# Kernel tuning notes

Measured on AMD Instinct MI355X. Metric: run time of the kernel, lower is better.

The kernel has to match this reference:

```python
import jax, jax.numpy as jnp
import numpy as np
import math

H = 8
KAPPA = 20.0
STAGES = 10
BN_EPS = 1e-5


def _l2norm(x, axis):
    return x / (1e-6 + jnp.linalg.norm(x, axis=axis, keepdims=True))


def _pmms(node, query_feature, mu0):
    # node: (b,c,n)  query_feature: (b,n,c)  mu0: (1,c,k)
    b = node.shape[0]
    mu = jnp.broadcast_to(mu0, (b, mu0.shape[1], mu0.shape[2]))

    def step(mu, _):
        z = jax.nn.softmax(KAPPA * jnp.einsum('bcn,bck->bnk', node, mu), axis=2)
        z = z / (1e-6 + z.sum(axis=1, keepdims=True))
        mu = _l2norm(jnp.einsum('bcn,bnk->bck', node, z), axis=1)
        return mu, None

    mu, _ = jax.lax.scan(step, mu, None, length=STAGES)
    mu = jax.lax.stop_gradient(mu)  # torch.no_grad in EM
    P = jax.lax.stop_gradient(
        jax.nn.softmax(jnp.einsum('bnc,bck->bnk', query_feature, mu), axis=2))
    return P, mu


def _conv2d_same(x, w):
    return jax.lax.conv_general_dilated(
        x, w, (1, 1), 'SAME', dimension_numbers=('NCHW', 'OIHW', 'NCHW'))


def _node_weight(x, cw1, cb1, g, be, cw2, cb2):
    # x: (b, n, ch) with n a perfect square
    b, n, ch = x.shape
    w = int(math.isqrt(n))
    y = x.transpose(0, 2, 1).reshape(b * ch, 1, w, w)
    y = _conv2d_same(y, cw1) + cb1[None, :, None, None]
    # eval-mode BatchNorm2d (running_mean=0, running_var=1)
    y = g[None, :, None, None] * (y / jnp.sqrt(1.0 + BN_EPS)) + be[None, :, None, None]
    y = jax.nn.relu(y)
    y = _conv2d_same(y, cw2) + cb2[None, :, None, None]
    y = jax.nn.sigmoid(y)
    y = y.reshape(b, ch, n).transpose(0, 2, 1)
    return x * y


def setup_inputs() -> dict:
    key = jax.random.key(0)
    ks = jax.random.split(key, 16)
    b, n, d = 16, 1024, 256
    s = 0.02
    mu_a = _l2norm(jax.random.normal(ks[6], (1, d, 5), jnp.float32) * math.sqrt(2.0 / 5), axis=1)
    mu_b = _l2norm(jax.random.normal(ks[7], (1, d, 2), jnp.float32) * math.sqrt(2.0 / 2), axis=1)
    return {
        'query': jax.random.normal(ks[0], (b, n, d), jnp.float32),
        'key': jax.random.normal(ks[1], (b, n, d), jnp.float32),
        'value': jax.random.normal(ks[2], (b, n), jnp.float32),
        'lamda': jax.random.uniform(ks[3], (1,), jnp.float32),
        'W0': jax.random.normal(ks[4], (d, d), jnp.float32) * s,
        'b0': jnp.zeros((d,), jnp.float32),
        'W1': jax.random.normal(ks[5], (d, d), jnp.float32) * s,
        'b1': jnp.zeros((d,), jnp.float32),
        'mu_a': mu_a,
        'mu_b': mu_b,
        'nw1_w1': jax.random.normal(ks[8], (16, 1, 3, 3), jnp.float32) * 0.1,
        'nw1_b1': jnp.zeros((16,), jnp.float32),
        'nw1_g': jnp.ones((16,), jnp.float32),
        'nw1_be': jnp.zeros((16,), jnp.float32),
        'nw1_w2': jax.random.normal(ks[9], (1, 16, 3, 3), jnp.float32) * 0.1,
        'nw1_b2': jnp.zeros((1,), jnp.float32),
        'nw2_w1': jax.random.normal(ks[10], (16, 1, 3, 3), jnp.float32) * 0.1,
        'nw2_b1': jnp.zeros((16,), jnp.float32),
        'nw2_g': jnp.ones((16,), jnp.float32),
        'nw2_be': jnp.zeros((16,), jnp.float32),
        'nw2_w2': jax.random.normal(ks[11], (1, 16, 3, 3), jnp.float32) * 0.1,
        'nw2_b2': jnp.zeros((1,), jnp.float32),
    }


def reference(query, key, value, lamda, W0, b0, W1, b1, mu_a, mu_b,
              nw1_w1, nw1_b1, nw1_g, nw1_be, nw1_w2, nw1_b2,
              nw2_w1, nw2_b1, nw2_g, nw2_be, nw2_w2, nw2_b2):
    b, n, d = query.shape
    dk = d // H
    scale = 1.0 / math.sqrt(dk)
    # linear projections, split heads: (b,H,n,dk)
    q_l = (query @ W0.T + b0).reshape(b, n, H, dk).transpose(0, 2, 1, 3)
    k_l = (key @ W1.T + b1).reshape(b, n, H, dk).transpose(0, 2, 1, 3)
    v = value[:, None, :, None]  # (b,1,n,1) broadcast over heads
    # global path: value-weighted mean key, elementwise multiply-reduce, relu
    key_global = jnp.mean(k_l * v, axis=-2, keepdims=True)  # (b,H,1,dk)
    whole = jax.nn.relu(jnp.sum(q_l * key_global, axis=-1, keepdims=True) * scale)
    whole = jnp.mean(whole, axis=-3)  # (b,n,1)
    # local path: standard softmax attention with scalar values (dropout eval=identity)
    scores = jnp.einsum('bhqd,bhkd->bhqk', q_l, k_l) * scale
    p_attn = jax.nn.softmax(scores, axis=-1)
    part = jnp.einsum('bhqk,bk->bhq', p_attn, value)[..., None]  # (b,H,n,1)
    part = jnp.mean(part, axis=-3)  # (b,n,1)
    f = (1.0 - lamda) * part + lamda * whole
    # PMMs prototype clustering
    qT = query.transpose(0, 2, 1)  # (b,c,n)
    P1, m1 = _pmms(qT, query, mu_a)   # (b,n,5), (b,c,5)
    P2, _ = _pmms(m1, query, mu_b)    # (b,n,2)
    q1 = _node_weight(P1, nw1_w1, nw1_b1, nw1_g, nw1_be, nw1_w2, nw1_b2)
    q2 = _node_weight(P2, nw2_w1, nw2_b1, nw2_g, nw2_be, nw2_w2, nw2_b2)
    # tree_drop eval=identity
    return jnp.concatenate((f, q1, q2), axis=-1)  # (b,n,8)
```

## Files before the change

### kernel.cpp

```cpp
#include <hip/hip_runtime.h>
#include <hip/hip_bf16.h>
#include <math.h>

#define NN 1024
#define ND 256
#define PSTRIDE 1288

typedef __hip_bfloat16 bf;
__device__ __forceinline__ float bf2f(bf h) { return __bfloat162float(h); }

typedef __attribute__((ext_vector_type(8))) short bf16x8;
typedef __attribute__((ext_vector_type(4))) float f32x4;

__device__ __forceinline__ float wave_reduce_sum(float v) {
#pragma unroll
    for (int off = 32; off > 0; off >>= 1) v += __shfl_down(v, off, 64);
    return v;
}
__device__ __forceinline__ float wave_allreduce_sum(float v) {
#pragma unroll
    for (int off = 1; off < 64; off <<= 1) v += __shfl_xor(v, off, 64);
    return v;
}

__global__ void zero_k(float* __restrict__ out) {
    int i = blockIdx.x * 1024 + threadIdx.x;
    out[(size_t)i * 8] = 0.f;
}

__global__ __launch_bounds__(256) void gemm2_k(
    const float* __restrict__ Aq, const float* __restrict__ Ak,
    const float* __restrict__ W0, const float* __restrict__ b0v,
    const float* __restrict__ W1, const float* __restrict__ b1v,
    bf* __restrict__ QL, bf* __restrict__ KL)
{
    const float* A; const float* Bw; const float* bias; bf* C;
    if (blockIdx.z == 0) { A = Aq; Bw = W0; bias = b0v; C = QL; }
    else                 { A = Ak; Bw = W1; bias = b1v; C = KL; }
    __shared__ short Ahi[4 * 64 * 8],  Alo[4 * 64 * 8];
    __shared__ short Bhi[16 * 64 * 8], Blo[16 * 64 * 8];
    const int t = threadIdx.x;
    const int wave = t >> 6, lane = t & 63;
    const int m0 = blockIdx.x * 64;

    f32x4 acc[4][4];
#pragma unroll
    for (int m = 0; m < 4; m++)
#pragma unroll
        for (int n = 0; n < 4; n++)
#pragma unroll
            for (int r = 0; r < 4; r++) acc[m][n][r] = 0.f;

    for (int k0 = 0; k0 < 256; k0 += 32) {
        __syncthreads();
        {
            int fm = t >> 6, ls = t & 63;
            const float* src = A + (size_t)(m0 + fm * 16 + (ls & 15)) * 256 + k0 + ((ls >> 4) * 8);
            float4 x = *(const float4*)src;
            float4 y = *(const float4*)(src + 4);
            float v[8] = {x.x, x.y, x.z, x.w, y.x, y.y, y.z, y.w};
            short h[8], l8[8];
#pragma unroll
            for (int j = 0; j < 8; j++) {
                bf hb = __float2bfloat16(v[j]);
                float hf = __bfloat162float(hb);
                bf lb = __float2bfloat16(v[j] - hf);
                h[j] = *(short*)&hb; l8[j] = *(short*)&lb;
            }
            *(bf16x8*)&Ahi[t * 8] = *(bf16x8*)h;
            *(bf16x8*)&Alo[t * 8] = *(bf16x8*)l8;
        }
#pragma unroll
        for (int i = 0; i < 4; i++) {
            int idx = t + i * 256;
            int nf = idx >> 6, ls = idx & 63;
            const float* src = Bw + (size_t)(nf * 16 + (ls & 15)) * 256 + k0 + ((ls >> 4) * 8);
            float4 x = *(const float4*)src;
            float4 y = *(const float4*)(src + 4);
            float v[8] = {x.x, x.y, x.z, x.w, y.x, y.y, y.z, y.w};
            short h[8], l8[8];
#pragma unroll
            for (int j = 0; j < 8; j++) {
                bf hb = __float2bfloat16(v[j]);
                float hf = __bfloat162float(hb);
                bf lb = __float2bfloat16(v[j] - hf);
                h[j] = *(short*)&hb; l8[j] = *(short*)&lb;
            }
            *(bf16x8*)&Bhi[idx * 8] = *(bf16x8*)h;
            *(bf16x8*)&Blo[idx * 8] = *(bf16x8*)l8;
        }
        __syncthreads();
        bf16x8 ah[4], al[4], bh[4], bl[4];
#pragma unroll
        for (int m = 0; m < 4; m++) {
            ah[m] = *(const bf16x8*)&Ahi[(m * 64 + lane) * 8];
            al[m] = *(const bf16x8*)&Alo[(m * 64 + lane) * 8];
        }
#pragma unroll
        for (int n = 0; n < 4; n++) {
            int nf = wave * 4 + n;
            bh[n] = *(const bf16x8*)&Bhi[(nf * 64 + lane) * 8];
            bl[n] = *(const bf16x8*)&Blo[(nf * 64 + lane) * 8];
        }
#pragma unroll
        for (int m = 0; m < 4; m++)
#pragma unroll
            for (int n = 0; n < 4; n++) {
                acc[m][n] = __builtin_amdgcn_mfma_f32_16x16x32_bf16(ah[m], bh[n], acc[m][n], 0, 0, 0);
                acc[m][n] = __builtin_amdgcn_mfma_f32_16x16x32_bf16(ah[m], bl[n], acc[m][n], 0, 0, 0);
                acc[m][n] = __builtin_amdgcn_mfma_f32_16x16x32_bf16(al[m], bh[n], acc[m][n], 0, 0, 0);
            }
    }
#pragma unroll
    for (int n = 0; n < 4; n++) {
        int col = (wave * 4 + n) * 16 + (lane & 15);
        float bv = bias[col];
#pragma unroll
        for (int m = 0; m < 4; m++) {
            int row = m0 + m * 16 + (lane >> 4) * 4;
#pragma unroll
            for (int r = 0; r < 4; r++) {
                bf hv = __float2bfloat16(acc[m][n][r] + bv);
                C[(size_t)(row + r) * 256 + col] = hv;
            }
        }
    }
}

__global__ __launch_bounds__(256) void attn3_k(
    const bf* __restrict__ QL, const bf* __restrict__ KL,
    const float* __restrict__ value, const float* __restrict__ lamda,
    float* __restrict__ out)
{
    const int bh = blockIdx.x; const int b = bh >> 3, h = bh & 7;
    const int t = threadIdx.x;
    const int wave = t >> 6, lane = t & 63;
    const int q0 = blockIdx.y * 256 + wave * 64;
    const float scale = 0.17677669529663687f;

    __shared__ bf Kf[128 * 32];
    __shared__ float vv[128];

    bf16x8 qf[4];
    {
        const bf* qbase = QL + ((size_t)b * NN) * ND + h * 32 + (lane >> 4) * 8;
#pragma unroll
        for (int m = 0; m < 4; m++)
            qf[m] = *(const bf16x8*)(qbase + (size_t)(q0 + m * 16 + (lane & 15)) * ND);
    }
    f32x4 lsum[4], vacc[4], wacc[4];
#pragma unroll
    for (int m = 0; m < 4; m++)
#pragma unroll
        for (int r = 0; r < 4; r++) { lsum[m][r] = 0.f; vacc[m][r] = 0.f; wacc[m][r] = 0.f; }

    const bf* kbase = KL + ((size_t)b * NN) * ND + h * 32;
    for (int kt = 0; kt < 8; kt++) {
        const int k0 = kt * 128;
        __syncthreads();
#pragma unroll
        for (int i = 0; i < 2; i++) {
            int f = t + i * 256;
            int row = ((f >> 6) << 4) + (f & 15);
            int chunk = (f >> 4) & 3;
            *(bf16x8*)&Kf[f * 8] = *(const bf16x8*)(kbase + (size_t)(k0 + row) * ND + chunk * 8);
        }
        if (t < 128) vv[t] = value[(size_t)b * NN + k0 + t];
        __syncthreads();
#pragma unroll
        for (int s = 0; s < 8; s++) {
            bf16x8 bfr = *(const bf16x8*)&Kf[(s * 64 + lane) * 8];
            float vcol = vv[s * 16 + (lane & 15)];
#pragma unroll
            for (int m = 0; m < 4; m++) {
                f32x4 acc = {0.f, 0.f, 0.f, 0.f};
                acc = __builtin_amdgcn_mfma_f32_16x16x32_bf16(qf[m], bfr, acc, 0, 0, 0);
#pragma unroll
                for (int r = 0; r < 4; r++) {
                    float sraw = acc[r];
                    float p = __expf(sraw * scale);
                    lsum[m][r] += p;
                    vacc[m][r] += p * vcol;
                    wacc[m][r] += sraw * vcol;
                }
            }
        }
    }
    const float lam = lamda[0];
#pragma unroll
    for (int m = 0; m < 4; m++)
#pragma unroll
        for (int r = 0; r < 4; r++) {
            float ls = lsum[m][r], va = vacc[m][r], wa = wacc[m][r];
#pragma unroll
            for (int off = 1; off < 16; off <<= 1) {
                ls += __shfl_xor(ls, off, 64);
                va += __shfl_xor(va, off, 64);
                wa += __shfl_xor(wa, off, 64);
            }
            if ((lane & 15) == 0) {
                int q = q0 + m * 16 + (lane >> 4) * 4 + r;
                float part = va / ls;
                float whole = fmaxf(wa * scale * (1.0f / 1024.0f), 0.f);
                float f = ((1.f - lam) * part + lam * whole) * 0.125f;
                atomicAdd(&out[((size_t)b * NN + q) * 8], f);
            }
        }
}

__global__ __launch_bounds__(256) void pmms_a_k(
    const float* __restrict__ query, const float* __restrict__ mu0a,
    const float* __restrict__ pin, float* __restrict__ pout, int stage)
{
    __shared__ float qs[64 * 260];
    __shared__ float muT[5 * 256];
    __shared__ float z_s[64][8];
    __shared__ float red[32];
    int chunk = blockIdx.x, b = blockIdx.y;
    int t = threadIdx.x;
    int wave = t >> 6, lane = t & 63;

    {
        const float* qg = query + ((size_t)b * NN + chunk * 64) * ND;
        for (int i = t; i < 4096; i += 256) {
            int row = i >> 6, c4 = (i & 63) * 4;
            *(float4*)&qs[row * 260 + c4] = *(const float4*)&qg[(size_t)row * ND + c4];
        }
    }

    if (stage == 0) {
        for (int idx = t; idx < 1280; idx += 256)
            muT[idx] = mu0a[(idx & 255) * 5 + (idx >> 8)];
    } else {
        float mr[5] = {0,0,0,0,0};
        float cs[5] = {0,0,0,0,0};
        for (int ch = 0; ch < 16; ch++) {
            const float* pb = pin + ((size_t)(b * 16 + ch)) * PSTRIDE;
#pragma unroll
            for (int k = 0; k < 5; k++) mr[k] += pb[k * 256 + t];
#pragma unroll
            for (int k = 0; k < 5; k++) cs[k] += pb[1280 + k];
        }
#pragma unroll
        for (int k = 0; k < 5; k++) mr[k] *= 1.0f / (1e-6f + cs[k]);
#pragma unroll
        for (int k = 0; k < 5; k++) {
            float s = wave_reduce_sum(mr[k] * mr[k]);
            if (lane == 0) red[wave * 5 + k] = s;
        }
        __syncthreads();
        if (t < 5) red[20 + t] = 1.0f / (1e-6f + sqrtf(red[t] + red[5 + t] + red[10 + t] + red[15 + t]));
        __syncthreads();
#pragma unroll
        for (int k = 0; k < 5; k++) muT[k * 256 + t] = mr[k] * red[20 + k];
    }
    __syncthreads();

    int n_local = t >> 2, part = t & 3;
    const float* qrow = &qs[n_local * 260 + part * 64];
    float lg[5] = {0,0,0,0,0};
#pragma unroll
    for (int c4 = 0; c4 < 64; c4 += 4) {
        float4 qv = *(const float4*)&qrow[c4];
#pragma unroll
        for (int k = 0; k < 5; k++) {
            float4 mv = *(const float4*)&muT[k * 256 + part * 64 + c4];
            lg[k] += qv.x*mv.x + qv.y*mv.y + qv.z*mv.z + qv.w*mv.w;
        }
    }
#pragma unroll
    for (int k = 0; k < 5; k++) {
        lg[k] += __shfl_xor(lg[k], 1, 64);
        lg[k] += __shfl_xor(lg[k], 2, 64);
    }
    float mx = lg[0];
#pragma unroll
    for (int k = 1; k < 5; k++) mx = fmaxf(mx, lg[k]);
    float e[5], ssum = 0.f;
#pragma unroll
    for (int k = 0; k < 5; k++) { e[k] = expf(20.0f * (lg[k] - mx)); ssum += e[k]; }
    float is = 1.0f / ssum;
    if (part == 0) {
#pragma unroll
        for (int k = 0; k < 5; k++) z_s[n_local][k] = e[k] * is;
    }
    __syncthreads();

    float pa[5] = {0,0,0,0,0};
#pragma unroll 4
    for (int nl = 0; nl < 64; nl++) {
        float qv = qs[nl * 260 + t];
        float4 z4 = *(const float4*)&z_s[nl][0];
        float z4v = z_s[nl][4];
        pa[0] += qv * z4.x; pa[1] += qv * z4.y; pa[2] += qv * z4.z;
        pa[3] += qv * z4.w; pa[4] += qv * z4v;
    }
    float* pb = pout + ((size_t)(b * 16 + chunk)) * PSTRIDE;
#pragma unroll
    for (int k = 0; k < 5; k++) pb[k * 256 + t] = pa[k];
    if (t < 5) {
        float s = 0.f;
        for (int nl = 0; nl < 64; nl++) s += z_s[nl][t];
        pb[1280 + t] = s;
    }
}

__global__ __launch_bounds__(64) void pmms_b_k(
    const float* __restrict__ pin, const float* __restrict__ mu0b,
    float* __restrict__ m1_ws, float* __restrict__ mu2_ws)
{
    int b = blockIdx.x, lane = threadIdx.x;
    float nd[5][4];
    float cs[5] = {0,0,0,0,0};
#pragma unroll
    for (int n = 0; n < 5; n++)
#pragma unroll
        for (int j = 0; j < 4; j++) nd[n][j] = 0.f;
    for (int ch = 0; ch < 16; ch++) {
        const float* pb = pin + ((size_t)(b * 16 + ch)) * PSTRIDE;
#pragma unroll
        for (int n = 0; n < 5; n++)
#pragma unroll
            for (int j = 0; j < 4; j++) nd[n][j] += pb[n * 256 + lane + 64 * j];
#pragma unroll
        for (int n = 0; n < 5; n++) cs[n] += pb[1280 + n];
    }
#pragma unroll
    for (int n = 0; n < 5; n++) {
        float inv = 1.0f / (1e-6f + cs[n]);
        float sq = 0.f;
#pragma unroll
        for (int j = 0; j < 4; j++) { nd[n][j] *= inv; sq += nd[n][j] * nd[n][j]; }
        float s = wave_allreduce_sum(sq);
        float nr = 1.0f / (1e-6f + sqrtf(s));
#pragma unroll
        for (int j = 0; j < 4; j++) {
            nd[n][j] *= nr;
            m1_ws[((size_t)b * 5 + n) * 256 + lane + 64 * j] = nd[n][j];
        }
    }
    float mu[2][4];
#pragma unroll
    for (int k = 0; k < 2; k++)
#pragma unroll
        for (int j = 0; j < 4; j++) mu[k][j] = mu0b[(lane + 64 * j) * 2 + k];
    for (int stage = 0; stage < 10; stage++) {
        float z[5][2];
        float colsum0 = 0.f, colsum1 = 0.f;
#pragma unroll
        for (int n = 0; n < 5; n++) {
            float l0 = 0.f, l1 = 0.f;
#pragma unroll
            for (int j = 0; j < 4; j++) { l0 += nd[n][j] * mu[0][j]; l1 += nd[n][j] * mu[1][j]; }
            l0 = wave_allreduce_sum(l0);
            l1 = wave_allreduce_sum(l1);
            float a0 = 20.0f * l0, a1 = 20.0f * l1;
            float mxv = fmaxf(a0, a1);
            float e0 = expf(a0 - mxv), e1 = expf(a1 - mxv);
            float inv = 1.0f / (e0 + e1);
            z[n][0] = e0 * inv; z[n][1] = e1 * inv;
            colsum0 += z[n][0]; colsum1 += z[n][1];
        }
        float i0 = 1.0f / (1e-6f + colsum0), i1 = 1.0f / (1e-6f + colsum1);
#pragma unroll
        for (int k = 0; k < 2; k++) {
            float iv = k ? i1 : i0;
            float sq = 0.f;
            float nm[4];
#pragma unroll
            for (int j = 0; j < 4; j++) {
                float v = 0.f;
#pragma unroll
                for (int n = 0; n < 5; n++) v += nd[n][j] * z[n][k];
                v *= iv;
                nm[j] = v; sq += v * v;
            }
            float s = wave_allreduce_sum(sq);
            float nr = 1.0f / (1e-6f + sqrtf(s));
#pragma unroll
            for (int j = 0; j < 4; j++) mu[k][j] = nm[j] * nr;
        }
    }
#pragma unroll
    for (int k = 0; k < 2; k++)
#pragma unroll
        for (int j = 0; j < 4; j++) mu2_ws[((size_t)b * 2 + k) * 256 + lane + 64 * j] = mu[k][j];
}

__global__ __launch_bounds__(256) void pmap_k(
    const float* __restrict__ query, const float* __restrict__ m1_ws,
    const float* __restrict__ mu2_ws, float* __restrict__ P1, float* __restrict__ P2)
{
    __shared__ float ms[7 * 256];
    int b = blockIdx.y;
    int t = threadIdx.x;
    int n = blockIdx.x * 256 + t;
    for (int idx = t; idx < 1280; idx += 256) ms[idx] = m1_ws[(size_t)b * 1280 + idx];
    for (int idx = t; idx < 512; idx += 256) ms[1280 + idx] = mu2_ws[(size_t)b * 512 + idx];
    __syncthreads();
    const float* qrow = query + ((size_t)b * NN + n) * ND;
    float lg[7] = {0,0,0,0,0,0,0};
    for (int c4 = 0; c4 < 256; c4 += 4) {
        float4 qv = *(const float4*)&qrow[c4];
#pragma unroll
        for (int k = 0; k < 7; k++) {
            float4 mv = *(const float4*)&ms[k * 256 + c4];
            lg[k] += qv.x*mv.x + qv.y*mv.y + qv.z*mv.z + qv.w*mv.w;
        }
    }
    float mx = lg[0];
#pragma unroll
    for (int k = 1; k < 5; k++) mx = fmaxf(mx, lg[k]);
    float e[5], ssum = 0.f;
#pragma unroll
    for (int k = 0; k < 5; k++) { e[k] = expf(lg[k] - mx); ssum += e[k]; }
    float is = 1.0f / ssum;
#pragma unroll
    for (int k = 0; k < 5; k++) P1[((size_t)b * 5 + k) * NN + n] = e[k] * is;
    float mx2 = fmaxf(lg[5], lg[6]);
    float e0 = expf(lg[5] - mx2), e1 = expf(lg[6] - mx2);
    float inv = 1.0f / (e0 + e1);
    P2[((size_t)b * 2 + 0) * NN + n] = e0 * inv;
    P2[((size_t)b * 2 + 1) * NN + n] = e1 * inv;
}

__global__ __launch_bounds__(1024) void nwconv_k(
    const float* __restrict__ P1, const float* __restrict__ P2,
    const float* __restrict__ w1a, const float* __restrict__ b1a,
    const float* __restrict__ ga,  const float* __restrict__ bea,
    const float* __restrict__ w2a, const float* __restrict__ b2a,
    const float* __restrict__ w1b, const float* __restrict__ b1b,
    const float* __restrict__ gb,  const float* __restrict__ beb,
    const float* __restrict__ w2b, const float* __restrict__ b2b,
    float* __restrict__ out)
{
    __shared__ float img[34 * 34];
    __shared__ float mid[16][34 * 34];
    __shared__ float w1s[144], w2s[144], bs[16], gs[16], bes[16], b2s[1];
    int ch = blockIdx.x, b = blockIdx.y;
    int t = threadIdx.x;
    int i = t >> 5, j = t & 31;
    const float* xsrc = (ch < 5) ? &P1[((size_t)b * 5 + ch) * NN]
                                 : &P2[((size_t)b * 2 + (ch - 5)) * NN];
    if (t < 144) { w1s[t] = (ch < 5 ? w1a : w1b)[t]; w2s[t] = (ch < 5 ? w2a : w2b)[t]; }
    if (t >= 256 && t < 272) {
        int y = t - 256;
        bs[y] = (ch < 5 ? b1a : b1b)[y];
        gs[y] = (ch < 5 ? ga : gb)[y];
        bes[y] = (ch < 5 ? bea : beb)[y];
    }
    if (t == 512) b2s[0] = (ch < 5 ? b2a : b2b)[0];
    for (int idx = t; idx < 1156; idx += 1024) img[idx] = 0.f;
    for (int idx = t; idx < 16 * 1156; idx += 1024) ((float*)mid)[idx] = 0.f;
    __syncthreads();
    float xv = xsrc[t];
    img[(i + 1) * 34 + (j + 1)] = xv;
    __syncthreads();
    float r[9];
#pragma unroll
    for (int dy = 0; dy < 3; dy++)
#pragma unroll
        for (int dx = 0; dx < 3; dx++)
            r[dy * 3 + dx] = img[(i + dy) * 34 + (j + dx)];
    const float bninv = rsqrtf(1.0f + 1e-5f);
#pragma unroll
    for (int oc = 0; oc < 16; oc++) {
        float a = 0.f;
#pragma unroll
        for (int q2 = 0; q2 < 9; q2++) a += w1s[oc * 9 + q2] * r[q2];
        a += bs[oc];
        a = gs[oc] * (a * bninv) + bes[oc];
        a = fmaxf(a, 0.f);
        mid[oc][(i + 1) * 34 + (j + 1)] = a;
    }
    __syncthreads();
    float acc2 = b2s[0];
#pragma unroll
    for (int oc = 0; oc < 16; oc++)
#pragma unroll
        for (int dy = 0; dy < 3; dy++)
#pragma unroll
            for (int dx = 0; dx < 3; dx++)
                acc2 += w2s[oc * 9 + dy * 3 + dx] * mid[oc][(i + dy) * 34 + (j + dx)];
    float sig = 1.0f / (1.0f + expf(-acc2));
    out[((size_t)(b * NN + t)) * 8 + 1 + ch] = xv * sig;
}

extern "C" void kernel_launch(void* const* d_in, const int* in_sizes, int n_in,
                              void* d_out, int out_size, void* d_ws, size_t ws_size,
                              hipStream_t stream) {
    const float* query = (const float*)d_in[0];
    const float* key   = (const float*)d_in[1];
    const float* value = (const float*)d_in[2];
    const float* lamda = (const float*)d_in[3];
    const float* W0 = (const float*)d_in[4];
    const float* b0 = (const float*)d_in[5];
    const float* W1 = (const float*)d_in[6];
    const float* b1 = (const float*)d_in[7];
    const float* mu_a = (const float*)d_in[8];
    const float* mu_b = (const float*)d_in[9];
    const float* nw1_w1 = (const float*)d_in[10];
    const float* nw1_b1 = (const float*)d_in[11];
    const float* nw1_g  = (const float*)d_in[12];
    const float* nw1_be = (const float*)d_in[13];
    const float* nw1_w2 = (const float*)d_in[14];
    const float* nw1_b2 = (const float*)d_in[15];
    const float* nw2_w1 = (const float*)d_in[16];
    const float* nw2_b1 = (const float*)d_in[17];
    const float* nw2_g  = (const float*)d_in[18];
    const float* nw2_be = (const float*)d_in[19];
    const float* nw2_w2 = (const float*)d_in[20];
    const float* nw2_b2 = (const float*)d_in[21];
    float* out = (float*)d_out;

    bf* QLb = (bf*)d_ws;
    bf* KLb = (bf*)((char*)d_ws + ((size_t)8 << 20));
    float* PA   = (float*)d_ws;
    float* PB   = PA + (size_t)16 * 16 * PSTRIDE;
    float* m1w  = PB + (size_t)16 * 16 * PSTRIDE;
    float* mu2w = m1w + (size_t)16 * 1280;
    float* P1w  = mu2w + (size_t)16 * 512;
    float* P2w  = P1w + (size_t)16 * 5 * 1024;

    zero_k<<<16, 1024, 0, stream>>>(out);
    gemm2_k<<<dim3(256, 1, 2), 256, 0, stream>>>(query, key, W0, b0, W1, b1, QLb, KLb);
    attn3_k<<<dim3(128, 4), 256, 0, stream>>>(QLb, KLb, value, lamda, out);
    for (int s = 0; s < 10; s++) {
        const float* pin = (s & 1) ? PA : PB;
        float* pout      = (s & 1) ? PB : PA;
        pmms_a_k<<<dim3(16, 16), 256, 0, stream>>>(query, mu_a, pin, pout, s);
    }
    pmms_b_k<<<16, 64, 0, stream>>>(PB, mu_b, m1w, mu2w);
    pmap_k<<<dim3(4, 16), 256, 0, stream>>>(query, m1w, mu2w, P1w, P2w);
    nwconv_k<<<dim3(7, 16), 1024, 0, stream>>>(P1w, P2w,
                                    nw1_w1, nw1_b1, nw1_g, nw1_be, nw1_w2, nw1_b2,
                                    nw2_w1, nw2_b1, nw2_g, nw2_be, nw2_w2, nw2_b2, out);
}
```

Measured before the change: 397.1 us.

## Fold softmax scale into Q projection, halve attention tile, split PMMs mu update

The Q projection output is pre-scaled by scale*log2(e) so the attention inner loop can use exp2 directly, and the whole-path constant becomes ln2/1024 to match. The attention kernel now gives each wave 32 queries instead of 64 and launches twice as many blocks, trading more K reloads for more occupancy. The PMMs EM loop is split into a small per-batch mu normalization kernel and a z-accumulation kernel over 32 chunks of 32 rows. The z kernel reads query straight from global memory instead of staging it in LDS, so the mu reduction is no longer repeated in every block, at the cost of twice as many kernel launches.

```diff
diff --git a/kernel.cpp b/kernel.cpp
--- a/kernel.cpp
+++ b/kernel.cpp
@@ -4,13 +4,16 @@
 
 #define NN 1024
 #define ND 256
+#define NCH 32
 #define PSTRIDE 1288
 
 typedef __hip_bfloat16 bf;
-__device__ __forceinline__ float bf2f(bf h) { return __bfloat162float(h); }
 
 typedef __attribute__((ext_vector_type(8))) short bf16x8;
 typedef __attribute__((ext_vector_type(4))) float f32x4;
+
+#define QL_ALPHA 0.25503486216f
+#define WHOLE_LN2 0.6931471805599453f
 
 __device__ __forceinline__ float wave_reduce_sum(float v) {
 #pragma unroll
@@ -34,9 +37,9 @@
     const float* __restrict__ W1, const float* __restrict__ b1v,
     bf* __restrict__ QL, bf* __restrict__ KL)
 {
-    const float* A; const float* Bw; const float* bias; bf* C;
-    if (blockIdx.z == 0) { A = Aq; Bw = W0; bias = b0v; C = QL; }
-    else                 { A = Ak; Bw = W1; bias = b1v; C = KL; }
+    const float* A; const float* Bw; const float* bias; bf* C; float alpha;
+    if (blockIdx.z == 0) { A = Aq; Bw = W0; bias = b0v; C = QL; alpha = QL_ALPHA; }
+    else                 { A = Ak; Bw = W1; bias = b1v; C = KL; alpha = 1.0f; }
     __shared__ short Ahi[4 * 64 * 8],  Alo[4 * 64 * 8];
     __shared__ short Bhi[16 * 64 * 8], Blo[16 * 64 * 8];
     const int t = threadIdx.x;
@@ -120,14 +123,14 @@
             int row = m0 + m * 16 + (lane >> 4) * 4;
 #pragma unroll
             for (int r = 0; r < 4; r++) {
-                bf hv = __float2bfloat16(acc[m][n][r] + bv);
+                bf hv = __float2bfloat16((acc[m][n][r] + bv) * alpha);
                 C[(size_t)(row + r) * 256 + col] = hv;
             }
         }
     }
 }
 
-__global__ __launch_bounds__(256) void attn3_k(
+__global__ __launch_bounds__(256) void attn4_k(
     const bf* __restrict__ QL, const bf* __restrict__ KL,
     const float* __restrict__ value, const float* __restrict__ lamda,
     float* __restrict__ out)
@@ -135,22 +138,21 @@
     const int bh = blockIdx.x; const int b = bh >> 3, h = bh & 7;
     const int t = threadIdx.x;
     const int wave = t >> 6, lane = t & 63;
-    const int q0 = blockIdx.y * 256 + wave * 64;
-    const float scale = 0.17677669529663687f;
+    const int q0 = blockIdx.y * 128 + wave * 32;
 
     __shared__ bf Kf[128 * 32];
     __shared__ float vv[128];
 
-    bf16x8 qf[4];
+    bf16x8 qf[2];
     {
         const bf* qbase = QL + ((size_t)b * NN) * ND + h * 32 + (lane >> 4) * 8;
 #pragma unroll
-        for (int m = 0; m < 4; m++)
+        for (int m = 0; m < 2; m++)
             qf[m] = *(const bf16x8*)(qbase + (size_t)(q0 + m * 16 + (lane & 15)) * ND);
     }
-    f32x4 lsum[4], vacc[4], wacc[4];
-#pragma unroll
-    for (int m = 0; m < 4; m++)
+    f32x4 lsum[2], vacc[2], wacc[2];
+#pragma unroll
+    for (int m = 0; m < 2; m++)
 #pragma unroll
         for (int r = 0; r < 4; r++) { lsum[m][r] = 0.f; vacc[m][r] = 0.f; wacc[m][r] = 0.f; }
 
@@ -172,13 +174,13 @@
             bf16x8 bfr = *(const bf16x8*)&Kf[(s * 64 + lane) * 8];
             float vcol = vv[s * 16 + (lane & 15)];
 #pragma unroll
-            for (int m = 0; m < 4; m++) {
+            for (int m = 0; m < 2; m++) {
                 f32x4 acc = {0.f, 0.f, 0.f, 0.f};
                 acc = __builtin_amdgcn_mfma_f32_16x16x32_bf16(qf[m], bfr, acc, 0, 0, 0);
 #pragma unroll
                 for (int r = 0; r < 4; r++) {
                     float sraw = acc[r];
-                    float p = __expf(sraw * scale);
+                    float p = exp2f(sraw);
                     lsum[m][r] += p;
                     vacc[m][r] += p * vcol;
                     wacc[m][r] += sraw * vcol;
@@ -188,7 +190,7 @@
     }
     const float lam = lamda[0];
 #pragma unroll
-    for (int m = 0; m < 4; m++)
+    for (int m = 0; m < 2; m++)
 #pragma unroll
         for (int r = 0; r < 4; r++) {
             float ls = lsum[m][r], va = vacc[m][r], wa = wacc[m][r];
@@ -201,106 +203,110 @@
             if ((lane & 15) == 0) {
                 int q = q0 + m * 16 + (lane >> 4) * 4 + r;
                 float part = va / ls;
-                float whole = fmaxf(wa * scale * (1.0f / 1024.0f), 0.f);
+                float whole = fmaxf(wa * (WHOLE_LN2 / 1024.0f), 0.f);
                 float f = ((1.f - lam) * part + lam * whole) * 0.125f;
                 atomicAdd(&out[((size_t)b * NN + q) * 8], f);
             }
         }
 }
 
-__global__ __launch_bounds__(256) void pmms_a_k(
+__global__ __launch_bounds__(256) void mu_k(
+    const float* __restrict__ pin, float* __restrict__ muG)
+{
+    __shared__ float red[32];
+    const int b = blockIdx.x, t = threadIdx.x;
+    const int wave = t >> 6, lane = t & 63;
+    float mr[5] = {0,0,0,0,0};
+    float cs[5] = {0,0,0,0,0};
+    for (int ch = 0; ch < NCH; ch++) {
+        const float* pb = pin + ((size_t)(b * NCH + ch)) * PSTRIDE;
+#pragma unroll
+        for (int k = 0; k < 5; k++) mr[k] += pb[k * 256 + t];
+#pragma unroll
+        for (int k = 0; k < 5; k++) cs[k] += pb[1280 + k];
+    }
+#pragma unroll
+    for (int k = 0; k < 5; k++) mr[k] *= 1.0f / (1e-6f + cs[k]);
+#pragma unroll
+    for (int k = 0; k < 5; k++) {
+        float s = wave_reduce_sum(mr[k] * mr[k]);
+        if (lane == 0) red[wave * 5 + k] = s;
+    }
+    __syncthreads();
+    if (t < 5) red[20 + t] = 1.0f / (1e-6f + sqrtf(red[t] + red[5 + t] + red[10 + t] + red[15 + t]));
+    __syncthreads();
+#pragma unroll
+    for (int k = 0; k < 5; k++)
+        muG[(size_t)b * 1280 + k * 256 + t] = mr[k] * red[20 + k];
+}
+
+__global__ __launch_bounds__(256) void zacc_k(
     const float* __restrict__ query, const float* __restrict__ mu0a,
-    const float* __restrict__ pin, float* __restrict__ pout, int stage)
-{
-    __shared__ float qs[64 * 260];
+    const float* __restrict__ muG, float* __restrict__ pout, int stage)
+{
     __shared__ float muT[5 * 256];
-    __shared__ float z_s[64][8];
-    __shared__ float red[32];
-    int chunk = blockIdx.x, b = blockIdx.y;
-    int t = threadIdx.x;
-    int wave = t >> 6, lane = t & 63;
-
-    {
-        const float* qg = query + ((size_t)b * NN + chunk * 64) * ND;
-        for (int i = t; i < 4096; i += 256) {
-            int row = i >> 6, c4 = (i & 63) * 4;
-            *(float4*)&qs[row * 260 + c4] = *(const float4*)&qg[(size_t)row * ND + c4];
-        }
-    }
+    __shared__ float z_s[32][8];
+    const int chunk = blockIdx.x, b = blockIdx.y;
+    const int t = threadIdx.x;
 
     if (stage == 0) {
         for (int idx = t; idx < 1280; idx += 256)
             muT[idx] = mu0a[(idx & 255) * 5 + (idx >> 8)];
     } else {
-        float mr[5] = {0,0,0,0,0};
-        float cs[5] = {0,0,0,0,0};
-        for (int ch = 0; ch < 16; ch++) {
-            const float* pb = pin + ((size_t)(b * 16 + ch)) * PSTRIDE;
-#pragma unroll
-            for (int k = 0; k < 5; k++) mr[k] += pb[k * 256 + t];
-#pragma unroll
-            for (int k = 0; k < 5; k++) cs[k] += pb[1280 + k];
-        }
-#pragma unroll
-        for (int k = 0; k < 5; k++) mr[k] *= 1.0f / (1e-6f + cs[k]);
+        for (int idx = t; idx < 1280; idx += 256)
+            muT[idx] = muG[(size_t)b * 1280 + idx];
+    }
+    __syncthreads();
+
+    const int n_local = t >> 3, part = t & 7;
+    {
+        const float* qrow = query + ((size_t)b * NN + chunk * 32 + n_local) * ND + part * 32;
+        float lg[5] = {0,0,0,0,0};
+#pragma unroll
+        for (int c4 = 0; c4 < 32; c4 += 4) {
+            float4 qv = *(const float4*)&qrow[c4];
+#pragma unroll
+            for (int k = 0; k < 5; k++) {
+                float4 mv = *(const float4*)&muT[k * 256 + part * 32 + c4];
+                lg[k] += qv.x*mv.x + qv.y*mv.y + qv.z*mv.z + qv.w*mv.w;
+            }
+        }
 #pragma unroll
         for (int k = 0; k < 5; k++) {
-            float s = wave_reduce_sum(mr[k] * mr[k]);
-            if (lane == 0) red[wave * 5 + k] = s;
-        }
-        __syncthreads();
-        if (t < 5) red[20 + t] = 1.0f / (1e-6f + sqrtf(red[t] + red[5 + t] + red[10 + t] + red[15 + t]));
-        __syncthreads();
-#pragma unroll
-        for (int k = 0; k < 5; k++) muT[k * 256 + t] = mr[k] * red[20 + k];
-    }
-    __syncthreads();
-
-    int n_local = t >> 2, part = t & 3;
-    const float* qrow = &qs[n_local * 260 + part * 64];
-    float lg[5] = {0,0,0,0,0};
-#pragma unroll
-    for (int c4 = 0; c4 < 64; c4 += 4) {
-        float4 qv = *(const float4*)&qrow[c4];
-#pragma unroll
-        for (int k = 0; k < 5; k++) {
-            float4 mv = *(const float4*)&muT[k * 256 + part * 64 + c4];
-            lg[k] += qv.x*mv.x + qv.y*mv.y + qv.z*mv.z + qv.w*mv.w;
-        }
-    }
-#pragma unroll
-    for (int k = 0; k < 5; k++) {
-        lg[k] += __shfl_xor(lg[k], 1, 64);
-        lg[k] += __shfl_xor(lg[k], 2, 64);
-    }
-    float mx = lg[0];
-#pragma unroll
-    for (int k = 1; k < 5; k++) mx = fmaxf(mx, lg[k]);
-    float e[5], ssum = 0.f;
-#pragma unroll
-    for (int k = 0; k < 5; k++) { e[k] = expf(20.0f * (lg[k] - mx)); ssum += e[k]; }
-    float is = 1.0f / ssum;
-    if (part == 0) {
-#pragma unroll
-        for (int k = 0; k < 5; k++) z_s[n_local][k] = e[k] * is;
+            lg[k] += __shfl_xor(lg[k], 1, 64);
+            lg[k] += __shfl_xor(lg[k], 2, 64);
+            lg[k] += __shfl_xor(lg[k], 4, 64);
+        }
+        float mx = lg[0];
+#pragma unroll
+        for (int k = 1; k < 5; k++) mx = fmaxf(mx, lg[k]);
+        float e[5], ssum = 0.f;
+#pragma unroll
+        for (int k = 0; k < 5; k++) { e[k] = expf(20.0f * (lg[k] - mx)); ssum += e[k]; }
+        float is = 1.0f / ssum;
+        if (part == 0) {
+#pragma unroll
+            for (int k = 0; k < 5; k++) z_s[n_local][k] = e[k] * is;
+        }
     }
     __syncthreads();
 
     float pa[5] = {0,0,0,0,0};
+    const float* qcol = query + ((size_t)b * NN + chunk * 32) * ND + t;
 #pragma unroll 4
-    for (int nl = 0; nl < 64; nl++) {
-        float qv = qs[nl * 260 + t];
+    for (int nl = 0; nl < 32; nl++) {
+        float qv = qcol[(size_t)nl * ND];
         float4 z4 = *(const float4*)&z_s[nl][0];
         float z4v = z_s[nl][4];
         pa[0] += qv * z4.x; pa[1] += qv * z4.y; pa[2] += qv * z4.z;
         pa[3] += qv * z4.w; pa[4] += qv * z4v;
     }
-    float* pb = pout + ((size_t)(b * 16 + chunk)) * PSTRIDE;
+    float* pb = pout + ((size_t)(b * NCH + chunk)) * PSTRIDE;
 #pragma unroll
     for (int k = 0; k < 5; k++) pb[k * 256 + t] = pa[k];
     if (t < 5) {
         float s = 0.f;
-        for (int nl = 0; nl < 64; nl++) s += z_s[nl][t];
+        for (int nl = 0; nl < 32; nl++) s += z_s[nl][t];
         pb[1280 + t] = s;
     }
 }
@@ -316,8 +322,8 @@
     for (int n = 0; n < 5; n++)
 #pragma unroll
         for (int j = 0; j < 4; j++) nd[n][j] = 0.f;
-    for (int ch = 0; ch < 16; ch++) {
-        const float* pb = pin + ((size_t)(b * 16 + ch)) * PSTRIDE;
+    for (int ch = 0; ch < NCH; ch++) {
+        const float* pb = pin + ((size_t)(b * NCH + ch)) * PSTRIDE;
 #pragma unroll
         for (int n = 0; n < 5; n++)
 #pragma unroll
@@ -516,19 +522,23 @@
     bf* QLb = (bf*)d_ws;
     bf* KLb = (bf*)((char*)d_ws + ((size_t)8 << 20));
     float* PA   = (float*)d_ws;
-    float* PB   = PA + (size_t)16 * 16 * PSTRIDE;
-    float* m1w  = PB + (size_t)16 * 16 * PSTRIDE;
+    float* PB   = PA + (size_t)16 * NCH * PSTRIDE;
+    float* m1w  = PB + (size_t)16 * NCH * PSTRIDE;
     float* mu2w = m1w + (size_t)16 * 1280;
     float* P1w  = mu2w + (size_t)16 * 512;
     float* P2w  = P1w + (size_t)16 * 5 * 1024;
+    float* muG  = P2w + (size_t)16 * 2 * 1024;
 
     zero_k<<<16, 1024, 0, stream>>>(out);
     gemm2_k<<<dim3(256, 1, 2), 256, 0, stream>>>(query, key, W0, b0, W1, b1, QLb, KLb);
-    attn3_k<<<dim3(128, 4), 256, 0, stream>>>(QLb, KLb, value, lamda, out);
-    for (int s = 0; s < 10; s++) {
+    attn4_k<<<dim3(128, 8), 256, 0, stream>>>(QLb, KLb, value, lamda, out);
+
+    zacc_k<<<dim3(NCH, 16), 256, 0, stream>>>(query, mu_a, muG, PA, 0);
+    for (int s = 1; s < 10; s++) {
         const float* pin = (s & 1) ? PA : PB;
         float* pout      = (s & 1) ? PB : PA;
-        pmms_a_k<<<dim3(16, 16), 256, 0, stream>>>(query, mu_a, pin, pout, s);
+        mu_k<<<16, 256, 0, stream>>>(pin, muG);
+        zacc_k<<<dim3(NCH, 16), 256, 0, stream>>>(query, mu_a, muG, pout, s);
     }
     pmms_b_k<<<16, 64, 0, stream>>>(PB, mu_b, m1w, mu2w);
     pmap_k<<<dim3(4, 16), 256, 0, stream>>>(query, m1w, mu2w, P1w, P2w);
```

Result: slower. 410.7 us (+3.4%).
